# Optimization experiments

Measured on AMD Instinct MI355X. Metric: run time of the kernel, lower is better.

## Reference

```python
import jax, jax.numpy as jnp
import numpy as np

MAX_LEN = 3

def _attention(h, enc, w1, b1, w2):
    # h: [B,H], enc: [B,S,H]
    B, S, H = enc.shape
    hs = jnp.broadcast_to(h[:, None, :], (B, S, H))
    x = jnp.tanh(jnp.concatenate([enc, hs], axis=-1) @ w1.T + b1)  # [B,S,H]
    e = (x @ w2.T)[..., 0]                                         # [B,S]
    alpha = jax.nn.softmax(e, axis=1)
    return jnp.einsum('bs,bsd->bd', alpha, enc)                    # [B,H]

def _gru_cell(x, h, w_ih, w_hh, b_ih, b_hh):
    # torch GRU gate order: r, z, n
    H = h.shape[-1]
    gi = x @ w_ih.T + b_ih   # [B,3H]
    gh = h @ w_hh.T + b_hh
    i_r, i_z, i_n = gi[:, :H], gi[:, H:2*H], gi[:, 2*H:]
    h_r, h_z, h_n = gh[:, :H], gh[:, H:2*H], gh[:, 2*H:]
    r = jax.nn.sigmoid(i_r + h_r)
    z = jax.nn.sigmoid(i_z + h_z)
    n = jnp.tanh(i_n + r * h_n)
    return (1.0 - z) * n + z * h

def setup_inputs() -> dict:
    key = jax.random.key(0)
    ks = jax.random.split(key, 16)
    B, S, H, DW = 1024, 40, 1024, 512
    V0 = V1 = 4000
    EMB_N = V0 + V1 + 1
    sc = lambda fan: 1.0 / np.sqrt(fan)
    inp = {
        'encoder_outputs': jax.random.normal(ks[0], (B, S, H), jnp.float32),
        'encoder_hidden': jax.random.normal(ks[1], (1, B, H), jnp.float32),
        'targets': jax.random.randint(ks[2], (MAX_LEN, B), 0, V0),
        'emb': jax.random.normal(ks[3], (EMB_N, DW), jnp.float32) * 0.02,
        'attn_w1': jax.random.normal(ks[4], (H, 2 * H), jnp.float32) * sc(2 * H),
        'attn_b1': jnp.zeros((H,), jnp.float32),
        'attn_w2': jax.random.normal(ks[5], (1, H), jnp.float32) * sc(H),
        'w_ih': jax.random.normal(ks[6], (3 * H, H + DW), jnp.float32) * sc(H),
        'w_hh': jax.random.normal(ks[7], (3 * H, H), jnp.float32) * sc(H),
        'b_ih': jnp.zeros((3 * H,), jnp.float32),
        'b_hh': jnp.zeros((3 * H,), jnp.float32),
        'out0_w': jax.random.normal(ks[8], (V0, H), jnp.float32) * sc(H),
        'out0_b': jnp.zeros((V0,), jnp.float32),
        'out1_w': jax.random.normal(ks[9], (V1, H), jnp.float32) * sc(H),
        'out1_b': jnp.zeros((V1,), jnp.float32),
    }
    return inp

def reference(encoder_outputs, encoder_hidden, targets, emb, attn_w1, attn_b1,
              attn_w2, w_ih, w_hh, b_ih, b_hh, out0_w, out0_b, out1_w, out1_b):
    B = encoder_outputs.shape[0]
    h = encoder_hidden[0]  # n_layers=1, unidirectional -> init state passthrough
    logs = []
    for t in range(MAX_LEN):
        context = _attention(h, encoder_outputs, attn_w1, attn_b1, attn_w2)
        if t == 0:
            it = jnp.zeros((B,), jnp.int32)
        elif t == 1:
            it = targets[0] + 1
        else:
            it = targets[t - 1] + 36
        x = jnp.concatenate([emb[it], context], axis=1)  # [B, DW+H]
        h = _gru_cell(x, h, w_ih, w_hh, b_ih, b_hh)
        if t == 0 or t == 2:
            logits = h @ out0_w.T + out0_b
        else:
            logits = h @ out1_w.T + out1_b
        logs.append(jax.nn.log_softmax(logits, axis=1))
    return jnp.stack(logs)  # [MAX_LEN, B, V]
```

## Files before the change

### kernel.cpp

```cpp
#include <hip/hip_runtime.h>
#include <hip/hip_bf16.h>
#include <math.h>

#define B_SZ 1024
#define S_SZ 40
#define H_SZ 1024
#define DW_SZ 512
#define V_SZ 4000
#define XW (DW_SZ + H_SZ)
#define NG (4 * H_SZ)

typedef __bf16 bf16x8 __attribute__((ext_vector_type(8)));
typedef float f32x4 __attribute__((ext_vector_type(4)));

__device__ __forceinline__ float fast_tanh(float x) {
    return 1.0f - 2.0f / (1.0f + __expf(2.0f * x));
}
__device__ __forceinline__ float fast_sigmoid(float x) {
    return 1.0f / (1.0f + __expf(-x));
}
__device__ __forceinline__ float bfraw2f(unsigned short u) {
    return __uint_as_float(((unsigned)u) << 16);
}

#define GLL16(gp, lp)                                                                \
    __builtin_amdgcn_global_load_lds((const __attribute__((address_space(1))) void*)(gp), \
                                     (__attribute__((address_space(3))) void*)(lp), 16, 0, 0)

template <int OB, int SWZ>
__global__ __launch_bounds__(256) void gemm_bt_mfma(
    const __hip_bfloat16* __restrict__ A, int lda,
    const __hip_bfloat16* __restrict__ W, int ldw,
    const float* __restrict__ bias,
    void* __restrict__ Cv, int ldc,
    int nbx, int N, int K) {
    __shared__ __align__(16) __hip_bfloat16 As[128 * 32];
    __shared__ __align__(16) __hip_bfloat16 Ws[128 * 32];
    const int tid = threadIdx.x;
    const int lane = tid & 63;
    const int wave = tid >> 6;

    int bid = blockIdx.x;
    if (SWZ) {
        const int cpx = gridDim.x >> 3;
        bid = (bid & 7) * cpx + (bid >> 3);
    }
    const int by = bid / nbx;
    const int bx = bid - by * nbx;
    const int bm = by * 128;
    const int bn = bx * 128;

    const int r0 = tid >> 2;
    const int kk = (tid & 3) * 8;
    const __hip_bfloat16* gA0 = A + (size_t)(bm + r0) * lda + kk;
    const __hip_bfloat16* gA1 = gA0 + (size_t)64 * lda;
    int wrow0 = bn + r0;      if (wrow0 > N - 1) wrow0 = N - 1;
    int wrow1 = bn + r0 + 64; if (wrow1 > N - 1) wrow1 = N - 1;
    const __hip_bfloat16* gW0 = W + (size_t)wrow0 * ldw + kk;
    const __hip_bfloat16* gW1 = W + (size_t)wrow1 * ldw + kk;
    char* As_c = (char*)As + tid * 16;
    char* Ws_c = (char*)Ws + tid * 16;

    const int wr = wave >> 1, wc = wave & 1;
    const int fr = lane & 15, fq = lane >> 4;
    const __hip_bfloat16* Ard = &As[(wr * 64 + fr) * 32 + fq * 8];
    const __hip_bfloat16* Wrd = &Ws[(wc * 64 + fr) * 32 + fq * 8];

    f32x4 acc[4][4] = {};

    for (int k0 = 0; k0 < K; k0 += 32) {
        __syncthreads();
        GLL16(gA0 + k0, As_c);
        GLL16(gA1 + k0, As_c + 4096);
        GLL16(gW0 + k0, Ws_c);
        GLL16(gW1 + k0, Ws_c + 4096);
        __syncthreads();

        bf16x8 af[4], bg[4];
#pragma unroll
        for (int i = 0; i < 4; ++i) {
            af[i] = *reinterpret_cast<const bf16x8*>(Ard + i * 16 * 32);
            bg[i] = *reinterpret_cast<const bf16x8*>(Wrd + i * 16 * 32);
        }
#pragma unroll
        for (int mi = 0; mi < 4; ++mi)
#pragma unroll
            for (int ni = 0; ni < 4; ++ni)
                acc[mi][ni] = __builtin_amdgcn_mfma_f32_16x16x32_bf16(af[mi], bg[ni], acc[mi][ni], 0, 0, 0);
    }

#pragma unroll
    for (int ni = 0; ni < 4; ++ni) {
        const int col = bn + wc * 64 + ni * 16 + fr;
        if (col >= N) continue;
        const float bb = bias ? bias[col] : 0.0f;
#pragma unroll
        for (int mi = 0; mi < 4; ++mi) {
            const int row0 = bm + wr * 64 + mi * 16 + fq * 4;
#pragma unroll
            for (int r = 0; r < 4; ++r) {
                const float v = acc[mi][ni][r] + bb;
                if (OB)
                    reinterpret_cast<__hip_bfloat16*>(Cv)[(size_t)(row0 + r) * ldc + col] = __float2bfloat16(v);
                else
                    reinterpret_cast<float*>(Cv)[(size_t)(row0 + r) * ldc + col] = v;
            }
        }
    }
}

__global__ __launch_bounds__(256) void gemm_dual_mfma(
    const __hip_bfloat16* __restrict__ A,
    const __hip_bfloat16* __restrict__ Wg,
    const __hip_bfloat16* __restrict__ Wo,
    const float* __restrict__ bias_cat,
    const float* __restrict__ ob,
    __hip_bfloat16* __restrict__ hg,
    float* __restrict__ logits,
    int full) {
    const int nbx = 64;
    const int bid = blockIdx.x;
    const int by = bid / nbx;
    const int bx = bid - by * nbx;
    const int bm = by * 128;
    const int bn = bx * 128;
    const int is_hg = (bn < NG);
    if (!full && is_hg) return;

    __shared__ __align__(16) __hip_bfloat16 As[128 * 32];
    __shared__ __align__(16) __hip_bfloat16 Ws[128 * 32];
    const int tid = threadIdx.x;
    const int lane = tid & 63;
    const int wave = tid >> 6;

    const __hip_bfloat16* Wb = is_hg ? Wg : Wo;
    const int coff = is_hg ? bn : bn - NG;
    const int nn = is_hg ? NG : V_SZ;

    const int r0 = tid >> 2;
    const int kk = (tid & 3) * 8;
    const __hip_bfloat16* gA0 = A + (size_t)(bm + r0) * H_SZ + kk;
    const __hip_bfloat16* gA1 = gA0 + (size_t)64 * H_SZ;
    int wrow0 = coff + r0;      if (wrow0 > nn - 1) wrow0 = nn - 1;
    int wrow1 = coff + r0 + 64; if (wrow1 > nn - 1) wrow1 = nn - 1;
    const __hip_bfloat16* gW0 = Wb + (size_t)wrow0 * H_SZ + kk;
    const __hip_bfloat16* gW1 = Wb + (size_t)wrow1 * H_SZ + kk;
    char* As_c = (char*)As + tid * 16;
    char* Ws_c = (char*)Ws + tid * 16;

    const int wr = wave >> 1, wc = wave & 1;
    const int fr = lane & 15, fq = lane >> 4;
    const __hip_bfloat16* Ard = &As[(wr * 64 + fr) * 32 + fq * 8];
    const __hip_bfloat16* Wrd = &Ws[(wc * 64 + fr) * 32 + fq * 8];

    f32x4 acc[4][4] = {};

    for (int k0 = 0; k0 < H_SZ; k0 += 32) {
        __syncthreads();
        GLL16(gA0 + k0, As_c);
        GLL16(gA1 + k0, As_c + 4096);
        GLL16(gW0 + k0, Ws_c);
        GLL16(gW1 + k0, Ws_c + 4096);
        __syncthreads();

        bf16x8 af[4], bg[4];
#pragma unroll
        for (int i = 0; i < 4; ++i) {
            af[i] = *reinterpret_cast<const bf16x8*>(Ard + i * 16 * 32);
            bg[i] = *reinterpret_cast<const bf16x8*>(Wrd + i * 16 * 32);
        }
#pragma unroll
        for (int mi = 0; mi < 4; ++mi)
#pragma unroll
            for (int ni = 0; ni < 4; ++ni)
                acc[mi][ni] = __builtin_amdgcn_mfma_f32_16x16x32_bf16(af[mi], bg[ni], acc[mi][ni], 0, 0, 0);
    }

#pragma unroll
    for (int ni = 0; ni < 4; ++ni) {
        const int cl = coff + wc * 64 + ni * 16 + fr;
        if (cl >= nn) continue;
        const float bb = is_hg ? bias_cat[cl] : ob[cl];
#pragma unroll
        for (int mi = 0; mi < 4; ++mi) {
            const int row0 = bm + wr * 64 + mi * 16 + fq * 4;
#pragma unroll
            for (int r = 0; r < 4; ++r) {
                const float v = acc[mi][ni][r] + bb;
                if (is_hg)
                    hg[(size_t)(row0 + r) * NG + cl] = __float2bfloat16(v);
                else
                    logits[(size_t)(row0 + r) * V_SZ + cl] = v;
            }
        }
    }
}

__global__ __launch_bounds__(256) void cast_f32_to_bf16(
    const float* __restrict__ src, long long sstride, int cols,
    __hip_bfloat16* __restrict__ dst, int nrows) {
    const int c4n = cols >> 2;
    const long long total4 = (long long)nrows * c4n;
    for (long long i = (long long)blockIdx.x * 256 + threadIdx.x; i < total4;
         i += (long long)gridDim.x * 256) {
        const long long r = i / c4n;
        const int c = (int)(i - r * c4n) << 2;
        const float4 v = *reinterpret_cast<const float4*>(src + r * sstride + c);
        union { ushort4 u; __hip_bfloat16 h[4]; } o;
        o.h[0] = __float2bfloat16(v.x); o.h[1] = __float2bfloat16(v.y);
        o.h[2] = __float2bfloat16(v.z); o.h[3] = __float2bfloat16(v.w);
        *reinterpret_cast<ushort4*>(dst + r * (long long)cols + c) = o.u;
    }
}

struct CastSeg { const float* src; long long sstride; int c4n; __hip_bfloat16* dst; long long n4; };
__global__ __launch_bounds__(256) void cast_all_kernel(CastSeg s0, CastSeg s1, CastSeg s2,
                                                       CastSeg s3, CastSeg s4, CastSeg s5) {
    const long long e0 = s0.n4, e1 = e0 + s1.n4, e2 = e1 + s2.n4,
                    e3 = e2 + s3.n4, e4 = e3 + s4.n4, e5 = e4 + s5.n4;
    for (long long i = (long long)blockIdx.x * 256 + threadIdx.x; i < e5;
         i += (long long)gridDim.x * 256) {
        CastSeg sg; long long li = i;
        if (i < e0) { sg = s0; }
        else if (i < e1) { sg = s1; li -= e0; }
        else if (i < e2) { sg = s2; li -= e1; }
        else if (i < e3) { sg = s3; li -= e2; }
        else if (i < e4) { sg = s4; li -= e3; }
        else { sg = s5; li -= e4; }
        const long long r = li / sg.c4n;
        const int c = (int)(li - r * sg.c4n) << 2;
        const float4 v = *reinterpret_cast<const float4*>(sg.src + r * sg.sstride + c);
        union { ushort4 u; __hip_bfloat16 h[4]; } o;
        o.h[0] = __float2bfloat16(v.x); o.h[1] = __float2bfloat16(v.y);
        o.h[2] = __float2bfloat16(v.z); o.h[3] = __float2bfloat16(v.w);
        *reinterpret_cast<ushort4*>(sg.dst + r * (long long)(sg.c4n << 2) + c) = o.u;
    }
}

__global__ __launch_bounds__(256) void build_bias_cat(
    const float* __restrict__ b1, const float* __restrict__ b_hh,
    float* __restrict__ dst) {
    const int j = blockIdx.x * 256 + threadIdx.x;
    dst[j] = (j < H_SZ) ? b1[j] : b_hh[j - H_SZ];
}

__global__ __launch_bounds__(256) void h_init_kernel(
    const float* __restrict__ enc_h, float* __restrict__ h, __hip_bfloat16* __restrict__ h_bf) {
    const int i = blockIdx.x * 256 + threadIdx.x;
    const float4 v = reinterpret_cast<const float4*>(enc_h)[i];
    reinterpret_cast<float4*>(h)[i] = v;
    union { ushort4 u; __hip_bfloat16 hh[4]; } o;
    o.hh[0] = __float2bfloat16(v.x); o.hh[1] = __float2bfloat16(v.y);
    o.hh[2] = __float2bfloat16(v.z); o.hh[3] = __float2bfloat16(v.w);
    reinterpret_cast<ushort4*>(h_bf)[i] = o.u;
}

__global__ __launch_bounds__(128) void emb_prefill_kernel(
    const float* __restrict__ emb,
    const int* __restrict__ targets,
    __hip_bfloat16* __restrict__ x0,
    __hip_bfloat16* __restrict__ x1,
    __hip_bfloat16* __restrict__ x2) {
    const int blk = blockIdx.x;
    const int t = blk >> 10;
    const int b = blk & 1023;
    const int tid = threadIdx.x;
    int it;
    __hip_bfloat16* x;
    if (t == 0) { it = 0; x = x0; }
    else if (t == 1) { it = targets[b] + 1; x = x1; }
    else { it = targets[B_SZ + b] + 36; x = x2; }
    float4 v = reinterpret_cast<const float4*>(emb + (size_t)it * DW_SZ)[tid];
    union { ushort4 u; __hip_bfloat16 h[4]; } o;
    o.h[0] = __float2bfloat16(v.x); o.h[1] = __float2bfloat16(v.y);
    o.h[2] = __float2bfloat16(v.z); o.h[3] = __float2bfloat16(v.w);
    reinterpret_cast<ushort4*>(x + (size_t)b * XW)[tid] = o.u;
}

__global__ __launch_bounds__(256) void attn_ctx_kernel(
    const __hip_bfloat16* __restrict__ enc,
    const __hip_bfloat16* __restrict__ enc_proj,
    const __hip_bfloat16* __restrict__ hg,
    const float* __restrict__ w2,
    __hip_bfloat16* __restrict__ x) {
    const int b = blockIdx.x;
    const int tid = threadIdx.x;
    const int lane = tid & 63, wave = tid >> 6;
    __shared__ float s_e[S_SZ];

    float hp[16], wv[16];
    const unsigned short* hgrow = reinterpret_cast<const unsigned short*>(hg) + (size_t)b * NG;
#pragma unroll
    for (int p = 0; p < 4; ++p) {
        const int base = p * 256 + lane * 4;
        ushort4 hu = *reinterpret_cast<const ushort4*>(hgrow + base);
        float4 wq = *reinterpret_cast<const float4*>(w2 + base);
        hp[p * 4 + 0] = bfraw2f(hu.x); hp[p * 4 + 1] = bfraw2f(hu.y);
        hp[p * 4 + 2] = bfraw2f(hu.z); hp[p * 4 + 3] = bfraw2f(hu.w);
        wv[p * 4 + 0] = wq.x; wv[p * 4 + 1] = wq.y;
        wv[p * 4 + 2] = wq.z; wv[p * 4 + 3] = wq.w;
    }

    const unsigned short* ep0 = reinterpret_cast<const unsigned short*>(enc_proj) + (size_t)b * S_SZ * H_SZ;
#pragma unroll 2
    for (int i = 0; i < 10; ++i) {
        const int s = wave + 4 * i;
        const unsigned short* row = ep0 + (size_t)s * H_SZ;
        float acc = 0.f;
#pragma unroll
        for (int p = 0; p < 4; ++p) {
            ushort4 eu = *reinterpret_cast<const ushort4*>(row + p * 256 + lane * 4);
            acc += fast_tanh(bfraw2f(eu.x) + hp[p * 4 + 0]) * wv[p * 4 + 0]
                 + fast_tanh(bfraw2f(eu.y) + hp[p * 4 + 1]) * wv[p * 4 + 1]
                 + fast_tanh(bfraw2f(eu.z) + hp[p * 4 + 2]) * wv[p * 4 + 2]
                 + fast_tanh(bfraw2f(eu.w) + hp[p * 4 + 3]) * wv[p * 4 + 3];
        }
#pragma unroll
        for (int off = 32; off > 0; off >>= 1) acc += __shfl_down(acc, off);
        if (lane == 0) s_e[s] = acc;
    }
    __syncthreads();

    float m = -1e30f;
    for (int s = 0; s < S_SZ; ++s) m = fmaxf(m, s_e[s]);
    float sum = 0.f;
    for (int s = 0; s < S_SZ; ++s) sum += __expf(s_e[s] - m);
    const float inv = 1.0f / sum;

    const ushort4* enc_b = reinterpret_cast<const ushort4*>(enc + (size_t)b * S_SZ * H_SZ);
    float4 acc = make_float4(0.f, 0.f, 0.f, 0.f);
    for (int s = 0; s < S_SZ; ++s) {
        const float a = __expf(s_e[s] - m) * inv;
        ushort4 ev = enc_b[s * 256 + tid];
        acc.x += a * bfraw2f(ev.x); acc.y += a * bfraw2f(ev.y);
        acc.z += a * bfraw2f(ev.z); acc.w += a * bfraw2f(ev.w);
    }
    union { ushort4 u; __hip_bfloat16 h[4]; } o;
    o.h[0] = __float2bfloat16(acc.x); o.h[1] = __float2bfloat16(acc.y);
    o.h[2] = __float2bfloat16(acc.z); o.h[3] = __float2bfloat16(acc.w);
    reinterpret_cast<ushort4*>(x + (size_t)b * XW + DW_SZ)[tid] = o.u;
}

__global__ __launch_bounds__(256) void gru_gate_kernel(
    const __hip_bfloat16* __restrict__ gi,
    const __hip_bfloat16* __restrict__ hg,
    float* __restrict__ h,
    __hip_bfloat16* __restrict__ h_bf) {
    const int idx = blockIdx.x * 256 + threadIdx.x;
    const int b = idx >> 10;
    const int j = idx & 1023;
    const unsigned short* gib = reinterpret_cast<const unsigned short*>(gi) + (size_t)b * 3 * H_SZ;
    const unsigned short* ghb = reinterpret_cast<const unsigned short*>(hg) + (size_t)b * NG + H_SZ;
    const float i_r = bfraw2f(gib[j]), i_z = bfraw2f(gib[H_SZ + j]), i_n = bfraw2f(gib[2 * H_SZ + j]);
    const float h_r = bfraw2f(ghb[j]), h_z = bfraw2f(ghb[H_SZ + j]), h_n = bfraw2f(ghb[2 * H_SZ + j]);
    const float r = fast_sigmoid(i_r + h_r);
    const float z = fast_sigmoid(i_z + h_z);
    const float n = fast_tanh(i_n + r * h_n);
    const float hv = (1.0f - z) * n + z * h[idx];
    h[idx] = hv;
    h_bf[idx] = __float2bfloat16(hv);
}

__global__ __launch_bounds__(256) void logsoftmax_kernel(float* __restrict__ buf) {
    const int b = blockIdx.x;
    const int tid = threadIdx.x;
    const int lane = tid & 63, wave = tid >> 6;
    __shared__ float s_red[4];
    __shared__ float s_bc;
    float* row = buf + (size_t)b * V_SZ;

    float m = -1e30f;
    for (int k = tid; k < V_SZ; k += 256) m = fmaxf(m, row[k]);
#pragma unroll
    for (int off = 32; off > 0; off >>= 1) m = fmaxf(m, __shfl_down(m, off));
    if (lane == 0) s_red[wave] = m;
    __syncthreads();
    if (tid == 0) s_bc = fmaxf(fmaxf(s_red[0], s_red[1]), fmaxf(s_red[2], s_red[3]));
    __syncthreads();
    m = s_bc;

    float sum = 0.f;
    for (int k = tid; k < V_SZ; k += 256) sum += expf(row[k] - m);
#pragma unroll
    for (int off = 32; off > 0; off >>= 1) sum += __shfl_down(sum, off);
    __syncthreads();
    if (lane == 0) s_red[wave] = sum;
    __syncthreads();
    if (tid == 0) s_bc = logf(s_red[0] + s_red[1] + s_red[2] + s_red[3]) + m;
    __syncthreads();
    const float ls = s_bc;

    for (int k = tid; k < V_SZ; k += 256) row[k] = row[k] - ls;
}

extern "C" void kernel_launch(void* const* d_in, const int* in_sizes, int n_in,
                              void* d_out, int out_size, void* d_ws, size_t ws_size,
                              hipStream_t stream) {
    const float* enc    = (const float*)d_in[0];
    const float* enc_h  = (const float*)d_in[1];
    const int*   tgt    = (const int*)d_in[2];
    const float* emb    = (const float*)d_in[3];
    const float* w1     = (const float*)d_in[4];
    const float* b1     = (const float*)d_in[5];
    const float* w2     = (const float*)d_in[6];
    const float* w_ih   = (const float*)d_in[7];
    const float* w_hh   = (const float*)d_in[8];
    const float* b_ih   = (const float*)d_in[9];
    const float* b_hh   = (const float*)d_in[10];
    const float* out0_w = (const float*)d_in[11];
    const float* out0_b = (const float*)d_in[12];
    const float* out1_w = (const float*)d_in[13];
    const float* out1_b = (const float*)d_in[14];
    float* out = (float*)d_out;

    char* wp = (char*)d_ws;
    auto carve = [&](size_t bytes) { char* p = wp; wp += (bytes + 255) & ~(size_t)255; return p; };
    __hip_bfloat16* enc_bf  = (__hip_bfloat16*)carve((size_t)B_SZ * S_SZ * H_SZ * 2);
    __hip_bfloat16* encp_bf = (__hip_bfloat16*)carve((size_t)B_SZ * S_SZ * H_SZ * 2);
    __hip_bfloat16* w1a_bf  = (__hip_bfloat16*)carve((size_t)H_SZ * H_SZ * 2);
    __hip_bfloat16* wcat_bf = (__hip_bfloat16*)carve((size_t)NG * H_SZ * 2);
    __hip_bfloat16* wih_bf  = (__hip_bfloat16*)carve((size_t)3 * H_SZ * XW * 2);
    __hip_bfloat16* o0_bf   = (__hip_bfloat16*)carve((size_t)V_SZ * H_SZ * 2);
    __hip_bfloat16* o1_bf   = (__hip_bfloat16*)carve((size_t)V_SZ * H_SZ * 2);
    float*          bias_cat= (float*)carve((size_t)NG * 4);
    float*          h       = (float*)carve((size_t)B_SZ * H_SZ * 4);
    __hip_bfloat16* h_bf    = (__hip_bfloat16*)carve((size_t)B_SZ * H_SZ * 2);
    __hip_bfloat16* hg_bf   = (__hip_bfloat16*)carve((size_t)B_SZ * NG * 2);
    __hip_bfloat16* x_bf[3];
    for (int t = 0; t < 3; ++t) x_bf[t] = (__hip_bfloat16*)carve((size_t)B_SZ * XW * 2);
    __hip_bfloat16* gi_bf   = (__hip_bfloat16*)carve((size_t)B_SZ * 3 * H_SZ * 2);

    cast_f32_to_bf16<<<2048, 256, 0, stream>>>(enc, H_SZ, H_SZ, enc_bf, B_SZ * S_SZ);
    {
        CastSeg s0{w1,            2 * H_SZ, H_SZ / 4, w1a_bf,                        (long long)H_SZ * H_SZ / 4};
        CastSeg s1{w1 + H_SZ,     2 * H_SZ, H_SZ / 4, wcat_bf,                       (long long)H_SZ * H_SZ / 4};
        CastSeg s2{w_hh,          H_SZ,     H_SZ / 4, wcat_bf + (size_t)H_SZ * H_SZ, (long long)3 * H_SZ * H_SZ / 4};
        CastSeg s3{w_ih,          XW,       XW / 4,   wih_bf,                        (long long)3 * H_SZ * XW / 4};
        CastSeg s4{out0_w,        H_SZ,     H_SZ / 4, o0_bf,                         (long long)V_SZ * H_SZ / 4};
        CastSeg s5{out1_w,        H_SZ,     H_SZ / 4, o1_bf,                         (long long)V_SZ * H_SZ / 4};
        cast_all_kernel<<<2048, 256, 0, stream>>>(s0, s1, s2, s3, s4, s5);
    }
    build_bias_cat<<<NG / 256, 256, 0, stream>>>(b1, b_hh, bias_cat);
    emb_prefill_kernel<<<3 * B_SZ, 128, 0, stream>>>(emb, tgt, x_bf[0], x_bf[1], x_bf[2]);
    h_init_kernel<<<(B_SZ * H_SZ / 4) / 256, 256, 0, stream>>>(enc_h, h, h_bf);

    gemm_bt_mfma<1, 1><<<(B_SZ * S_SZ / 128) * (H_SZ / 128), 256, 0, stream>>>(
        enc_bf, H_SZ, w1a_bf, H_SZ, nullptr, encp_bf, H_SZ, H_SZ / 128, H_SZ, H_SZ);

    gemm_bt_mfma<1, 0><<<(B_SZ / 128) * (NG / 128), 256, 0, stream>>>(
        h_bf, H_SZ, wcat_bf, H_SZ, bias_cat, hg_bf, NG, NG / 128, NG, H_SZ);

    for (int t = 0; t < 3; ++t) {
        attn_ctx_kernel<<<B_SZ, 256, 0, stream>>>(enc_bf, encp_bf, hg_bf, w2, x_bf[t]);

        gemm_bt_mfma<1, 0><<<(B_SZ / 128) * (3 * H_SZ / 128), 256, 0, stream>>>(
            x_bf[t], XW, wih_bf, XW, b_ih, gi_bf, 3 * H_SZ, 3 * H_SZ / 128, 3 * H_SZ, XW);

        gru_gate_kernel<<<(B_SZ * H_SZ) / 256, 256, 0, stream>>>(gi_bf, hg_bf, h, h_bf);

        float* logits = out + (size_t)t * B_SZ * V_SZ;
        const __hip_bfloat16* ow = (t == 1) ? o1_bf : o0_bf;
        const float* ob = (t == 1) ? out1_b : out0_b;
        gemm_dual_mfma<<<(B_SZ / 128) * 64, 256, 0, stream>>>(
            h_bf, wcat_bf, ow, bias_cat, ob, hg_bf, logits, (t < 2) ? 1 : 0);

        logsoftmax_kernel<<<B_SZ, 256, 0, stream>>>(logits);
    }
}
```

Measured before the change: 595.9 us.

## Use 256x256-tile triple-buffered MFMA GEMM for encoder projection

Replaces the 128x128-tile GEMM for the large encoder projection (40960x1024x1024) with a new 512-thread kernel that uses 256x256 tiles and a three-stage global-to-LDS pipeline with swizzled shared memory. Larger tiles raise arithmetic intensity and cut global traffic per FLOP, and the prefetch depth aims to hide load latency behind MFMA work. In exchange it uses 96KB of dynamic LDS and many accumulator registers, which may reduce occupancy. The dynamic LDS request may also need an explicit attribute to exceed default limits.

```diff
diff --git a/kernel.cpp b/kernel.cpp
--- a/kernel.cpp
+++ b/kernel.cpp
@@ -26,6 +26,105 @@
 #define GLL16(gp, lp)                                                                \
     __builtin_amdgcn_global_load_lds((const __attribute__((address_space(1))) void*)(gp), \
                                      (__attribute__((address_space(3))) void*)(lp), 16, 0, 0)
+
+__global__ __launch_bounds__(512, 2) void gemm_bt_256_pipe(
+    const __hip_bfloat16* __restrict__ A, int lda,
+    const __hip_bfloat16* __restrict__ W, int ldw,
+    __hip_bfloat16* __restrict__ C, int ldc,
+    int nbx, int K) {
+    extern __shared__ char smem[];
+    const int tid = threadIdx.x;
+    const int lane = tid & 63;
+    const int wave = tid >> 6;
+    const int wm = wave >> 2, wn = wave & 3;
+    const int fr = lane & 15, fq = lane >> 4;
+
+    int bid = blockIdx.x;
+    { const int cpx = gridDim.x >> 3; bid = (bid & 7) * cpx + (bid >> 3); }
+    const int by = bid / nbx;
+    const int bm = by * 256;
+    const int bn = (bid - by * nbx) * 256;
+
+    const int r0 = tid >> 2;
+    const int s0 = (tid & 3) ^ ((tid >> 3) & 3);
+    const __hip_bfloat16* gA0 = A + (size_t)(bm + r0) * lda + s0 * 8;
+    const __hip_bfloat16* gA1 = A + (size_t)(bm + r0 + 128) * lda + s0 * 8;
+    const __hip_bfloat16* gW0 = W + (size_t)(bn + r0) * ldw + s0 * 8;
+    const __hip_bfloat16* gW1 = W + (size_t)(bn + r0 + 128) * ldw + s0 * 8;
+    const int dst0 = tid * 16;
+
+    int aoff[8], boff[4];
+#pragma unroll
+    for (int mi = 0; mi < 8; ++mi) {
+        const int row = wm * 128 + mi * 16 + fr;
+        aoff[mi] = row * 64 + ((fq ^ ((row >> 1) & 3)) << 4);
+    }
+#pragma unroll
+    for (int ni = 0; ni < 4; ++ni) {
+        const int col = wn * 64 + ni * 16 + fr;
+        boff[ni] = 16384 + col * 64 + ((fq ^ ((col >> 1) & 3)) << 4);
+    }
+
+    const int NT = K >> 5;
+    f32x4 acc[8][4] = {};
+
+#define STAGE_T(t)                                                    \
+    do {                                                              \
+        char* sb = smem + ((t) % 3) * 32768;                          \
+        const int kk = (t) << 5;                                      \
+        GLL16(gA0 + kk, sb + dst0);                                   \
+        GLL16(gA1 + kk, sb + dst0 + 8192);                            \
+        GLL16(gW0 + kk, sb + 16384 + dst0);                           \
+        GLL16(gW1 + kk, sb + 16384 + dst0 + 8192);                    \
+    } while (0)
+
+    STAGE_T(0);
+    STAGE_T(1);
+    __builtin_amdgcn_sched_barrier(0);
+    asm volatile("s_waitcnt vmcnt(4)" ::: "memory");
+    __builtin_amdgcn_s_barrier();
+    __builtin_amdgcn_sched_barrier(0);
+
+    for (int t = 0; t < NT; ++t) {
+        if (t + 2 < NT) STAGE_T(t + 2);
+
+        const char* sb = smem + (t % 3) * 32768;
+        bf16x8 af[8], bg[4];
+#pragma unroll
+        for (int ni = 0; ni < 4; ++ni) bg[ni] = *reinterpret_cast<const bf16x8*>(sb + boff[ni]);
+#pragma unroll
+        for (int mi = 0; mi < 8; ++mi) af[mi] = *reinterpret_cast<const bf16x8*>(sb + aoff[mi]);
+
+        __builtin_amdgcn_s_setprio(1);
+#pragma unroll
+        for (int mi = 0; mi < 8; ++mi)
+#pragma unroll
+            for (int ni = 0; ni < 4; ++ni)
+                acc[mi][ni] = __builtin_amdgcn_mfma_f32_16x16x32_bf16(af[mi], bg[ni], acc[mi][ni], 0, 0, 0);
+        __builtin_amdgcn_s_setprio(0);
+
+        if (t != NT - 1) {
+            __builtin_amdgcn_sched_barrier(0);
+            if (t + 2 < NT) asm volatile("s_waitcnt vmcnt(4)" ::: "memory");
+            else            asm volatile("s_waitcnt vmcnt(0)" ::: "memory");
+            __builtin_amdgcn_s_barrier();
+            __builtin_amdgcn_sched_barrier(0);
+        }
+    }
+#undef STAGE_T
+
+#pragma unroll
+    for (int mi = 0; mi < 8; ++mi) {
+        const int row0 = bm + wm * 128 + mi * 16 + fq * 4;
+#pragma unroll
+        for (int ni = 0; ni < 4; ++ni) {
+            const int col = bn + wn * 64 + ni * 16 + fr;
+#pragma unroll
+            for (int r = 0; r < 4; ++r)
+                C[(size_t)(row0 + r) * ldc + col] = __float2bfloat16(acc[mi][ni][r]);
+        }
+    }
+}
 
 template <int OB, int SWZ>
 __global__ __launch_bounds__(256) void gemm_bt_mfma(
@@ -444,8 +543,8 @@
     emb_prefill_kernel<<<3 * B_SZ, 128, 0, stream>>>(emb, tgt, x_bf[0], x_bf[1], x_bf[2]);
     h_init_kernel<<<(B_SZ * H_SZ / 4) / 256, 256, 0, stream>>>(enc_h, h, h_bf);
 
-    gemm_bt_mfma<1, 1><<<(B_SZ * S_SZ / 128) * (H_SZ / 128), 256, 0, stream>>>(
-        enc_bf, H_SZ, w1a_bf, H_SZ, nullptr, encp_bf, H_SZ, H_SZ / 128, H_SZ, H_SZ);
+    gemm_bt_256_pipe<<<(B_SZ * S_SZ / 256) * (H_SZ / 256), 512, 3 * 32768, stream>>>(
+        enc_bf, H_SZ, w1a_bf, H_SZ, encp_bf, H_SZ, H_SZ / 256, H_SZ);
 
     gemm_bt_mfma<1, 0><<<(B_SZ / 128) * (NG / 128), 256, 0, stream>>>(
         h_bf, H_SZ, wcat_bf, H_SZ, bias_cat, hg_bf, NG, NG / 128, NG, H_SZ);
```

Result: faster. 568.2 us (-4.6%).
